# Kernel tuning notes

Measured on AMD Instinct MI355X. Metric: run time of the kernel, lower is better.

The kernel has to match this reference:

```python
import jax, jax.numpy as jnp
import numpy as np
import math

HIDDEN = 1024
HEADS = 16
HEAD_DIM = HIDDEN // HEADS
B, S = 4, 2048


def setup_inputs() -> dict:
    key = jax.random.key(0)
    ks = jax.random.split(key, 10)
    scale = 1.0 / math.sqrt(HIDDEN)
    inp = {
        "x": jax.random.normal(ks[0], (B, S, HIDDEN), dtype=jnp.float32),
        "attention_mask": jnp.ones((B, 1, 1, S), dtype=jnp.int32),
        "Wq": jax.random.normal(ks[1], (HIDDEN, HIDDEN), dtype=jnp.float32) * scale,
        "bq": jnp.zeros((HIDDEN,), dtype=jnp.float32),
        "Wk": jax.random.normal(ks[2], (HIDDEN, HIDDEN), dtype=jnp.float32) * scale,
        "bk": jnp.zeros((HIDDEN,), dtype=jnp.float32),
        "Wv": jax.random.normal(ks[3], (HIDDEN, HIDDEN), dtype=jnp.float32) * scale,
        "bv": jnp.zeros((HIDDEN,), dtype=jnp.float32),
        "Wo": jax.random.normal(ks[4], (HIDDEN, HIDDEN), dtype=jnp.float32) * scale,
        "bo": jnp.zeros((HIDDEN,), dtype=jnp.float32),
    }
    return inp


def reference(x, attention_mask, Wq, bq, Wk, bk, Wv, bv, Wo, bo):
    b, s, d = x.shape
    # nn.Linear: x @ W.T + b
    q = (x @ Wq.T + bq).reshape(b, s, HEADS, HEAD_DIM).transpose(0, 2, 1, 3)
    k = (x @ Wk.T + bk).reshape(b, s, HEADS, HEAD_DIM).transpose(0, 2, 1, 3)
    v = (x @ Wv.T + bv).reshape(b, s, HEADS, HEAD_DIM).transpose(0, 2, 1, 3)
    # explicit O(S^2) score matrix, as in the original
    scores = jnp.einsum("bhqd,bhkd->bhqk", q, k) / math.sqrt(HEAD_DIM)
    scores = jnp.where(attention_mask == 0, jnp.float32(-1e9), scores)
    attn = jax.nn.softmax(scores, axis=-1)
    # dropout(p=0.1) treated as identity (eval mode) for a deterministic reference
    out = jnp.einsum("bhqk,bhkd->bhqd", attn, v)
    out = out.transpose(0, 2, 1, 3).reshape(b, s, d)
    return out @ Wo.T + bo
```

## Files before the change

### kernel.cpp

```cpp
#include <hip/hip_runtime.h>
#include <math.h>

#define HID 1024
#define NH  16
#define HD  64
#define NB  4
#define SL  2048
#define MROWS (NB * SL)

typedef __attribute__((ext_vector_type(8))) short short8;
typedef __attribute__((ext_vector_type(4))) float f32x4;
typedef unsigned short ushort_t;
typedef unsigned int uint_t;

__device__ __forceinline__ uint_t f2bf(float x) {
    union { float f; uint_t u; } a; a.f = x;
    return (a.u + 0x7fffu + ((a.u >> 16) & 1u)) >> 16;
}

__device__ __forceinline__ void load_lds16(const void* g, void* l) {
    __builtin_amdgcn_global_load_lds(
        (const __attribute__((address_space(1))) void*)g,
        (__attribute__((address_space(3))) void*)l, 16, 0, 0);
}

__device__ __forceinline__ void gemm_core_bk64(
    const ushort_t* __restrict__ A, const ushort_t* __restrict__ B,
    const int m0, const int n0, ushort_t* As, ushort_t* Bs, f32x4 (&acc)[4][4])
{
    const int tid = threadIdx.x;
    const int w = tid >> 6, lane = tid & 63;
    const int wm = (w & 1) << 6, wn = (w >> 1) << 6;
    const int c = lane & 15, quad = lane >> 4;

    for (int k0 = 0; k0 < HID; k0 += 64) {
        __syncthreads();
        #pragma unroll
        for (int rd = 0; rd < 4; ++rd) {
            const int g = rd * 4 + w;
            const int idx = g * 64 + lane;
            const int r = idx >> 3, sc = idx & 7;
            const int dc = sc ^ (r & 7);
            load_lds16(&A[(size_t)(m0 + r) * HID + k0 + dc * 8], As + g * 512);
            load_lds16(&B[(size_t)(n0 + r) * HID + k0 + dc * 8], Bs + g * 512);
        }
        __syncthreads();

        #pragma unroll
        for (int ks = 0; ks < 2; ++ks) {
            short8 af[4], bf[4];
            #pragma unroll
            for (int i = 0; i < 4; ++i) {
                const int ra = wm + i * 16 + c;
                const int rb = wn + i * 16 + c;
                af[i] = *(const short8*)
                    &As[ra * 64 + ((((ks << 2) + quad) ^ (c & 7)) << 3)];
                bf[i] = *(const short8*)
                    &Bs[rb * 64 + ((((ks << 2) + quad) ^ (c & 7)) << 3)];
            }
            #pragma unroll
            for (int i = 0; i < 4; ++i)
                #pragma unroll
                for (int j = 0; j < 4; ++j)
                    acc[i][j] = __builtin_amdgcn_mfma_f32_16x16x32_bf16(
                        af[i], bf[j], acc[i][j], 0, 0, 0);
        }
    }
}

__global__ __launch_bounds__(256) void cvt_bf16_kernel(
    const float* __restrict__ x,
    const float* __restrict__ wq, const float* __restrict__ wk,
    const float* __restrict__ wv, const float* __restrict__ wo,
    ushort_t* __restrict__ xb, ushort_t* __restrict__ wqb,
    ushort_t* __restrict__ wkb, ushort_t* __restrict__ wvb,
    ushort_t* __restrict__ wob)
{
    const int seg = blockIdx.y;
    const float* src; ushort_t* dst;
    if (seg < 8)       { src = x + (size_t)seg * 1048576; dst = xb + (size_t)seg * 1048576; }
    else if (seg == 8) { src = wq; dst = wqb; }
    else if (seg == 9) { src = wk; dst = wkb; }
    else if (seg == 10){ src = wv; dst = wvb; }
    else               { src = wo; dst = wob; }
    const int i = (blockIdx.x * 256 + threadIdx.x) * 8;
    const float4 a = *(const float4*)&src[i];
    const float4 b = *(const float4*)&src[i + 4];
    uint4 o;
    o.x = f2bf(a.x) | (f2bf(a.y) << 16);
    o.y = f2bf(a.z) | (f2bf(a.w) << 16);
    o.z = f2bf(b.x) | (f2bf(b.y) << 16);
    o.w = f2bf(b.z) | (f2bf(b.w) << 16);
    *(uint4*)&dst[i] = o;
}

__global__ __launch_bounds__(256) void qkv_mfma_kernel(
    const ushort_t* __restrict__ xb,
    const ushort_t* __restrict__ wqb, const ushort_t* __restrict__ wkb,
    const ushort_t* __restrict__ wvb,
    const float* __restrict__ bq, const float* __restrict__ bk,
    const float* __restrict__ bv,
    ushort_t* __restrict__ qo, ushort_t* __restrict__ ko,
    ushort_t* __restrict__ vo)
{
    __shared__ __align__(16) ushort_t As[128 * 64];
    __shared__ __align__(16) ushort_t Bs[128 * 64];

    const int wsel = blockIdx.z;
    const ushort_t* W    = (wsel == 0) ? wqb : (wsel == 1) ? wkb : wvb;
    const float*    bias = (wsel == 0) ? bq  : (wsel == 1) ? bk  : bv;

    const int flat = blockIdx.x + (blockIdx.y << 3);
    const int xcd = flat & 7, s = flat >> 3;
    const int m0 = ((xcd << 3) + (s >> 3)) * 128;
    const int n0 = (s & 7) * 128;

    f32x4 acc[4][4];
    const f32x4 zero = {0.f, 0.f, 0.f, 0.f};
    #pragma unroll
    for (int i = 0; i < 4; ++i)
        #pragma unroll
        for (int j = 0; j < 4; ++j) acc[i][j] = zero;

    gemm_core_bk64(xb, W, m0, n0, As, Bs, acc);

    const int tid = threadIdx.x;
    const int w = tid >> 6, lane = tid & 63;
    const int wm = (w & 1) << 6, wn = (w >> 1) << 6;
    const int c = lane & 15, quad = lane >> 4;
    const float qscale = (wsel == 0) ? 0.18033688f : 1.0f;

    #pragma unroll
    for (int j = 0; j < 4; ++j) {
        const int n_g = n0 + wn + j * 16 + c;
        const float bj = bias[n_g];
        const int h = n_g >> 6, d = n_g & 63;
        #pragma unroll
        for (int i = 0; i < 4; ++i) {
            const int mbase = m0 + wm + i * 16 + quad * 4;
            const int b = mbase >> 11;
            const int sbase = mbase & (SL - 1);
            if (wsel == 2) {
                ushort4 pk;
                pk.x = (ushort_t)f2bf(acc[i][j][0] + bj);
                pk.y = (ushort_t)f2bf(acc[i][j][1] + bj);
                pk.z = (ushort_t)f2bf(acc[i][j][2] + bj);
                pk.w = (ushort_t)f2bf(acc[i][j][3] + bj);
                *(ushort4*)&vo[(((size_t)(b * NH + h) * HD) + d) * SL + sbase] = pk;
            } else {
                ushort_t* dst = (wsel == 0) ? qo : ko;
                #pragma unroll
                for (int reg = 0; reg < 4; ++reg) {
                    const float v = (acc[i][j][reg] + bj) * qscale;
                    dst[(((size_t)(b * NH + h) * SL) + sbase + reg) * HD + d] =
                        (ushort_t)f2bf(v);
                }
            }
        }
    }
}

__global__ __launch_bounds__(256, 4) void attn_mfma_kernel(
    const ushort_t* __restrict__ q, const ushort_t* __restrict__ k,
    const ushort_t* __restrict__ vt, const int* __restrict__ mask,
    ushort_t* __restrict__ ao)
{
    __shared__ __align__(16) ushort_t Ks[64 * 64];
    __shared__ __align__(16) ushort_t Vs[64 * 64];
    __shared__ __align__(16) ushort_t Ps[128 * 64];

    const int qt = blockIdx.x;
    const int bh = blockIdx.y;
    const int b = bh >> 4, h = bh & 15;
    const int tid = threadIdx.x;
    const int w = tid >> 6, lane = tid & 63;
    const int c = lane & 15, quad = lane >> 4;

    const ushort_t* qp = q  + (size_t)bh * SL * HD + (size_t)qt * 128 * HD;
    const ushort_t* kp = k  + (size_t)bh * SL * HD;
    const ushort_t* vp = vt + (size_t)bh * HD * SL;

    short8 qf[2][2];
    #pragma unroll
    for (int mi = 0; mi < 2; ++mi)
        #pragma unroll
        for (int ks = 0; ks < 2; ++ks)
            qf[mi][ks] = *(const short8*)&qp[(size_t)(w * 32 + mi * 16 + c) * HD
                                             + ks * 32 + quad * 8];

    const short one_bf = (short)0x3F80;
    const short8 ones8 = {one_bf, one_bf, one_bf, one_bf,
                          one_bf, one_bf, one_bf, one_bf};

    int kfo[4][2], vfo[4][2], pfo[2][2], pwo[2][4];
    #pragma unroll
    for (int ni = 0; ni < 4; ++ni)
        #pragma unroll
        for (int ks = 0; ks < 2; ++ks) {
            kfo[ni][ks] = (4 * c + ni) * 64 + (((ks * 4 + quad) ^ (c & 7)) << 3);
            vfo[ni][ks] = (ni * 16 + c) * 64 + (((ks * 4 + quad) ^ (c & 7)) << 3);
        }
    #pragma unroll
    for (int mi = 0; mi < 2; ++mi) {
        #pragma unroll
        for (int ks = 0; ks < 2; ++ks) {
            const int prow = w * 32 + mi * 16 + c;
            pfo[mi][ks] = prow * 64 + (((ks * 4 + quad) ^ (prow & 7)) << 3);
        }
        #pragma unroll
        for (int reg = 0; reg < 4; ++reg) {
            const int prow = w * 32 + mi * 16 + quad * 4 + reg;
            pwo[mi][reg] = prow * 64 + (((c >> 1) ^ (prow & 7)) * 8)
                           + ((c & 1) * 4);
        }
    }

    const ushort_t* kst[2]; const ushort_t* vst[2];
    #pragma unroll
    for (int rd = 0; rd < 2; ++rd) {
        const int t = (rd * 4 + w) * 64 + lane;
        const int r = t >> 3, sc = t & 7;
        kst[rd] = kp + (size_t)r * HD + (sc ^ ((r >> 2) & 7)) * 8;
        vst[rd] = vp + (size_t)r * SL + (sc ^ (r & 7)) * 8;
    }
    const int* mp = mask + b * SL + 4 * c;

    f32x4 oa[2][4];
    f32x4 oa1[2];
    const f32x4 zero = {0.f, 0.f, 0.f, 0.f};
    #pragma unroll
    for (int mi = 0; mi < 2; ++mi) {
        oa1[mi] = zero;
        #pragma unroll
        for (int ni = 0; ni < 4; ++ni) oa[mi][ni] = zero;
    }

    for (int kt = 0; kt < SL / 64; ++kt) {
        __syncthreads();
        load_lds16(kst[0], Ks + (0 * 4 + w) * 512);
        load_lds16(vst[0], Vs + (0 * 4 + w) * 512);
        load_lds16(kst[1], Ks + (1 * 4 + w) * 512);
        load_lds16(vst[1], Vs + (1 * 4 + w) * 512);
        kst[0] += 64 * HD; kst[1] += 64 * HD;
        vst[0] += 64;      vst[1] += 64;
        __syncthreads();

        const int4 mzv = *(const int4*)mp;
        mp += 64;
        float mb[4];
        mb[0] = (mzv.x == 0) ? -20000.f : 0.f;
        mb[1] = (mzv.y == 0) ? -20000.f : 0.f;
        mb[2] = (mzv.z == 0) ? -20000.f : 0.f;
        mb[3] = (mzv.w == 0) ? -20000.f : 0.f;

        f32x4 sf[2][4];
        #pragma unroll
        for (int mi = 0; mi < 2; ++mi)
            #pragma unroll
            for (int ni = 0; ni < 4; ++ni) {
                const f32x4 init = {mb[ni], mb[ni], mb[ni], mb[ni]};
                sf[mi][ni] = init;
            }
        __builtin_amdgcn_s_setprio(1);
        #pragma unroll
        for (int ni = 0; ni < 4; ++ni) {
            #pragma unroll
            for (int ks = 0; ks < 2; ++ks) {
                const short8 kf = *(const short8*)&Ks[kfo[ni][ks]];
                #pragma unroll
                for (int mi = 0; mi < 2; ++mi)
                    sf[mi][ni] = __builtin_amdgcn_mfma_f32_16x16x32_bf16(
                        qf[mi][ks], kf, sf[mi][ni], 0, 0, 0);
            }
        }
        __builtin_amdgcn_s_setprio(0);

        #pragma unroll
        for (int mi = 0; mi < 2; ++mi) {
            #pragma unroll
            for (int reg = 0; reg < 4; ++reg) {
                float p[4];
                #pragma unroll
                for (int ni = 0; ni < 4; ++ni)
                    p[ni] = __builtin_amdgcn_exp2f(sf[mi][ni][reg]);
                union { float f; uint_t u; } u0, u1, u2, u3;
                u0.f = p[0]; u1.f = p[1]; u2.f = p[2]; u3.f = p[3];
                uint2 pk;
                pk.x = __builtin_amdgcn_perm(u1.u, u0.u, 0x07060302u);
                pk.y = __builtin_amdgcn_perm(u3.u, u2.u, 0x07060302u);
                *(uint2*)&Ps[pwo[mi][reg]] = pk;
            }
        }

        short8 pf[2][2];
        #pragma unroll
        for (int mi = 0; mi < 2; ++mi)
            #pragma unroll
            for (int ks = 0; ks < 2; ++ks)
                pf[mi][ks] = *(const short8*)&Ps[pfo[mi][ks]];
        __builtin_amdgcn_s_setprio(1);
        #pragma unroll
        for (int ni = 0; ni < 4; ++ni) {
            #pragma unroll
            for (int ks = 0; ks < 2; ++ks) {
                const short8 vf = *(const short8*)&Vs[vfo[ni][ks]];
                #pragma unroll
                for (int mi = 0; mi < 2; ++mi)
                    oa[mi][ni] = __builtin_amdgcn_mfma_f32_16x16x32_bf16(
                        pf[mi][ks], vf, oa[mi][ni], 0, 0, 0);
            }
        }
        #pragma unroll
        for (int mi = 0; mi < 2; ++mi)
            #pragma unroll
            for (int ks = 0; ks < 2; ++ks)
                oa1[mi] = __builtin_amdgcn_mfma_f32_16x16x32_bf16(
                    pf[mi][ks], ones8, oa1[mi], 0, 0, 0);
        __builtin_amdgcn_s_setprio(0);
    }

    #pragma unroll
    for (int mi = 0; mi < 2; ++mi) {
        #pragma unroll
        for (int reg = 0; reg < 4; ++reg) {
            const float inv = 1.f / oa1[mi][reg];
            const int s_g = qt * 128 + w * 32 + mi * 16 + quad * 4 + reg;
            #pragma unroll
            for (int ni = 0; ni < 4; ++ni) {
                const int d = ni * 16 + c;
                ao[((size_t)(b * SL + s_g)) * HID + h * HD + d] =
                    (ushort_t)f2bf(oa[mi][ni][reg] * inv);
            }
        }
    }
}

__global__ __launch_bounds__(256, 4) void out_mfma_kernel(
    const ushort_t* __restrict__ aob, const ushort_t* __restrict__ wob,
    const float* __restrict__ bo, float* __restrict__ out)
{
    __shared__ __align__(16) ushort_t As[64 * 64];
    __shared__ __align__(16) ushort_t Bs[128 * 64];

    const int flat = blockIdx.x + (blockIdx.y << 3);
    const int xcd = flat & 7, s = flat >> 3;
    const int m0 = ((xcd << 4) + (s >> 3)) * 64;
    const int n0 = (s & 7) * 128;

    const int tid = threadIdx.x;
    const int w = tid >> 6, lane = tid & 63;
    const int wm = (w & 1) << 5;
    const int wn = (w >> 1) << 6;
    const int c = lane & 15, quad = lane >> 4;

    f32x4 acc[2][4];
    const f32x4 zero = {0.f, 0.f, 0.f, 0.f};
    #pragma unroll
    for (int i = 0; i < 2; ++i)
        #pragma unroll
        for (int j = 0; j < 4; ++j) acc[i][j] = zero;

    for (int k0 = 0; k0 < HID; k0 += 64) {
        __syncthreads();
        #pragma unroll
        for (int rd = 0; rd < 2; ++rd) {
            const int g = rd * 4 + w;
            const int idx = g * 64 + lane;
            const int r = idx >> 3, sc = idx & 7;
            const int dc = sc ^ (r & 7);
            load_lds16(&aob[(size_t)(m0 + r) * HID + k0 + dc * 8], As + g * 512);
        }
        #pragma unroll
        for (int rd = 0; rd < 4; ++rd) {
            const int g = rd * 4 + w;
            const int idx = g * 64 + lane;
            const int r = idx >> 3, sc = idx & 7;
            const int dc = sc ^ (r & 7);
            load_lds16(&wob[(size_t)(n0 + r) * HID + k0 + dc * 8], Bs + g * 512);
        }
        __syncthreads();

        #pragma unroll
        for (int ks = 0; ks < 2; ++ks) {
            short8 af[2], bf[4];
            #pragma unroll
            for (int i = 0; i < 2; ++i) {
                const int ra = wm + i * 16 + c;
                af[i] = *(const short8*)
                    &As[ra * 64 + ((((ks << 2) + quad) ^ (c & 7)) << 3)];
            }
            #pragma unroll
            for (int j = 0; j < 4; ++j) {
                const int rb = wn + j * 16 + c;
                bf[j] = *(const short8*)
                    &Bs[rb * 64 + ((((ks << 2) + quad) ^ (c & 7)) << 3)];
            }
            #pragma unroll
            for (int i = 0; i < 2; ++i)
                #pragma unroll
                for (int j = 0; j < 4; ++j)
                    acc[i][j] = __builtin_amdgcn_mfma_f32_16x16x32_bf16(
                        af[i], bf[j], acc[i][j], 0, 0, 0);
        }
    }

    #pragma unroll
    for (int j = 0; j < 4; ++j) {
        const int n_g = n0 + wn + j * 16 + c;
        const float bj = bo[n_g];
        #pragma unroll
        for (int i = 0; i < 2; ++i) {
            const int mbase = m0 + wm + i * 16 + quad * 4;
            #pragma unroll
            for (int reg = 0; reg < 4; ++reg)
                out[(size_t)(mbase + reg) * HID + n_g] = acc[i][j][reg] + bj;
        }
    }
}

extern "C" void kernel_launch(void* const* d_in, const int* in_sizes, int n_in,
                              void* d_out, int out_size, void* d_ws, size_t ws_size,
                              hipStream_t stream)
{
    const float* x    = (const float*)d_in[0];
    const int*   mask = (const int*)d_in[1];
    const float* Wq   = (const float*)d_in[2];
    const float* bq   = (const float*)d_in[3];
    const float* Wk   = (const float*)d_in[4];
    const float* bk   = (const float*)d_in[5];
    const float* Wv   = (const float*)d_in[6];
    const float* bv   = (const float*)d_in[7];
    const float* Wo   = (const float*)d_in[8];
    const float* bo   = (const float*)d_in[9];
    float* out = (float*)d_out;

    ushort_t* p = (ushort_t*)d_ws;
    ushort_t* xb  = p; p += (size_t)MROWS * HID;
    ushort_t* wqb = p; p += (size_t)HID * HID;
    ushort_t* wkb = p; p += (size_t)HID * HID;
    ushort_t* wvb = p; p += (size_t)HID * HID;
    ushort_t* wob = p; p += (size_t)HID * HID;
    ushort_t* qb  = p; p += (size_t)MROWS * HID;
    ushort_t* kb  = p; p += (size_t)MROWS * HID;
    ushort_t* vtb = p; p += (size_t)MROWS * HID;
    ushort_t* aob = p; p += (size_t)MROWS * HID;

    cvt_bf16_kernel<<<dim3(512, 12), 256, 0, stream>>>(
        x, Wq, Wk, Wv, Wo, xb, wqb, wkb, wvb, wob);
    qkv_mfma_kernel<<<dim3(8, 64, 3), 256, 0, stream>>>(
        xb, wqb, wkb, wvb, bq, bk, bv, qb, kb, vtb);
    attn_mfma_kernel<<<dim3(16, 64), 256, 0, stream>>>(
        qb, kb, vtb, mask, aob);
    out_mfma_kernel<<<dim3(8, 128), 256, 0, stream>>>(
        aob, wob, bo, out);
}
```

Before: 286.2 us.

## Enlarge output GEMM tile to 128x128 and double-buffer LDS loads

The output projection kernel now computes 128x128 tiles instead of 64x128, so each wave holds a 4x4 accumulator block and the grid is halved. LDS is double-buffered so the next K-slice's async global-to-LDS loads are issued while MFMAs run on the current slice, which also removes one barrier per step. The cost is higher register and LDS use, which lowers occupancy to 2 blocks per CU, and only 512 blocks remain to spread across the CUs. The loads for the next buffer are issued without an explicit wait before that buffer is consumed, relying on the barrier for completion, which is a correctness risk.

```diff
diff --git a/kernel.cpp b/kernel.cpp
--- a/kernel.cpp
+++ b/kernel.cpp
@@ -335,72 +335,81 @@
     }
 }
 
-__global__ __launch_bounds__(256, 4) void out_mfma_kernel(
+__global__ __launch_bounds__(256, 2) void out_mfma_kernel(
     const ushort_t* __restrict__ aob, const ushort_t* __restrict__ wob,
     const float* __restrict__ bo, float* __restrict__ out)
 {
-    __shared__ __align__(16) ushort_t As[64 * 64];
-    __shared__ __align__(16) ushort_t Bs[128 * 64];
+    __shared__ __align__(16) ushort_t As[2][128 * 64];
+    __shared__ __align__(16) ushort_t Bs[2][128 * 64];
 
     const int flat = blockIdx.x + (blockIdx.y << 3);
     const int xcd = flat & 7, s = flat >> 3;
-    const int m0 = ((xcd << 4) + (s >> 3)) * 64;
+    const int m0 = ((xcd << 3) + (s >> 3)) * 128;
     const int n0 = (s & 7) * 128;
 
     const int tid = threadIdx.x;
     const int w = tid >> 6, lane = tid & 63;
-    const int wm = (w & 1) << 5;
-    const int wn = (w >> 1) << 6;
+    const int wm = (w & 1) << 6, wn = (w >> 1) << 6;
     const int c = lane & 15, quad = lane >> 4;
 
-    f32x4 acc[2][4];
+    #pragma unroll
+    for (int rd = 0; rd < 4; ++rd) {
+        const int g = rd * 4 + w;
+        const int idx = g * 64 + lane;
+        const int r = idx >> 3, sc = idx & 7;
+        const int dc = sc ^ (r & 7);
+        load_lds16(&aob[(size_t)(m0 + r) * HID + dc * 8], As[0] + g * 512);
+        load_lds16(&wob[(size_t)(n0 + r) * HID + dc * 8], Bs[0] + g * 512);
+    }
+
+    f32x4 acc[4][4];
     const f32x4 zero = {0.f, 0.f, 0.f, 0.f};
     #pragma unroll
-    for (int i = 0; i < 2; ++i)
+    for (int i = 0; i < 4; ++i)
         #pragma unroll
         for (int j = 0; j < 4; ++j) acc[i][j] = zero;
 
-    for (int k0 = 0; k0 < HID; k0 += 64) {
-        __syncthreads();
-        #pragma unroll
-        for (int rd = 0; rd < 2; ++rd) {
-            const int g = rd * 4 + w;
-            const int idx = g * 64 + lane;
-            const int r = idx >> 3, sc = idx & 7;
-            const int dc = sc ^ (r & 7);
-            load_lds16(&aob[(size_t)(m0 + r) * HID + k0 + dc * 8], As + g * 512);
-        }
-        #pragma unroll
-        for (int rd = 0; rd < 4; ++rd) {
-            const int g = rd * 4 + w;
-            const int idx = g * 64 + lane;
-            const int r = idx >> 3, sc = idx & 7;
-            const int dc = sc ^ (r & 7);
-            load_lds16(&wob[(size_t)(n0 + r) * HID + k0 + dc * 8], Bs + g * 512);
-        }
-        __syncthreads();
-
-        #pragma unroll
-        for (int ks = 0; ks < 2; ++ks) {
-            short8 af[2], bf[4];
-            #pragma unroll
-            for (int i = 0; i < 2; ++i) {
-                const int ra = wm + i * 16 + c;
-                af[i] = *(const short8*)
-                    &As[ra * 64 + ((((ks << 2) + quad) ^ (c & 7)) << 3)];
-            }
-            #pragma unroll
-            for (int j = 0; j < 4; ++j) {
-                const int rb = wn + j * 16 + c;
-                bf[j] = *(const short8*)
-                    &Bs[rb * 64 + ((((ks << 2) + quad) ^ (c & 7)) << 3)];
-            }
-            #pragma unroll
-            for (int i = 0; i < 2; ++i)
-                #pragma unroll
-                for (int j = 0; j < 4; ++j)
-                    acc[i][j] = __builtin_amdgcn_mfma_f32_16x16x32_bf16(
-                        af[i], bf[j], acc[i][j], 0, 0, 0);
+    for (int k0 = 0; k0 < HID; k0 += 128) {
+        #pragma unroll
+        for (int half = 0; half < 2; ++half) {
+            const int kk = k0 + half * 64;
+            const int cur = half, nxt = half ^ 1;
+
+            __syncthreads();
+
+            if (kk + 64 < HID) {
+                #pragma unroll
+                for (int rd = 0; rd < 4; ++rd) {
+                    const int g = rd * 4 + w;
+                    const int idx = g * 64 + lane;
+                    const int r = idx >> 3, sc = idx & 7;
+                    const int dc = sc ^ (r & 7);
+                    load_lds16(&aob[(size_t)(m0 + r) * HID + kk + 64 + dc * 8],
+                               As[nxt] + g * 512);
+                    load_lds16(&wob[(size_t)(n0 + r) * HID + kk + 64 + dc * 8],
+                               Bs[nxt] + g * 512);
+                }
+            }
+
+            #pragma unroll
+            for (int ks = 0; ks < 2; ++ks) {
+                short8 af[4], bf[4];
+                #pragma unroll
+                for (int i = 0; i < 4; ++i) {
+                    const int ra = wm + i * 16 + c;
+                    const int rb = wn + i * 16 + c;
+                    af[i] = *(const short8*)
+                        &As[cur][ra * 64 + ((((ks << 2) + quad) ^ (c & 7)) << 3)];
+                    bf[i] = *(const short8*)
+                        &Bs[cur][rb * 64 + ((((ks << 2) + quad) ^ (c & 7)) << 3)];
+                }
+                #pragma unroll
+                for (int i = 0; i < 4; ++i)
+                    #pragma unroll
+                    for (int j = 0; j < 4; ++j)
+                        acc[i][j] = __builtin_amdgcn_mfma_f32_16x16x32_bf16(
+                            af[i], bf[j], acc[i][j], 0, 0, 0);
+            }
         }
     }
 
@@ -409,7 +418,7 @@
         const int n_g = n0 + wn + j * 16 + c;
         const float bj = bo[n_g];
         #pragma unroll
-        for (int i = 0; i < 2; ++i) {
+        for (int i = 0; i < 4; ++i) {
             const int mbase = m0 + wm + i * 16 + quad * 4;
             #pragma unroll
             for (int reg = 0; reg < 4; ++reg)
@@ -451,6 +460,6 @@
         xb, wqb, wkb, wvb, bq, bk, bv, qb, kb, vtb);
     attn_mfma_kernel<<<dim3(16, 64), 256, 0, stream>>>(
         qb, kb, vtb, mask, aob);
-    out_mfma_kernel<<<dim3(8, 128), 256, 0, stream>>>(
+    out_mfma_kernel<<<dim3(8, 64), 256, 0, stream>>>(
         aob, wob, bo, out);
 }
```

Result: faster. 280.4 us (-2.0%).
